# Performance work log

Measured on AMD Instinct MI355X. Metric: run time of the kernel, lower is better.

Reference implementation:

```python
import jax, jax.numpy as jnp
import numpy as np

NUM_NODES = 2   # number of iResNet blocks
H = 256         # internal_size
L = 4           # num_internal_layers (hidden Linear+ELU layers)
D = 2           # inp_size_linear (2D uv coords)
N = 1048576     # number of points (flattened 1024x1024 STMap grid)


def setup_inputs() -> dict:
    key = jax.random.key(0)
    ks = jax.random.split(key, 7)
    scale = 0.8 / np.sqrt(H)  # mimic lipschitz_correction (spectral norm <= 0.8)
    uv = jax.random.normal(ks[0], (N, D), jnp.float32)
    w_in = jax.random.normal(ks[1], (NUM_NODES, D, H), jnp.float32) * (0.8 / np.sqrt(D))
    b_in = jax.random.normal(ks[2], (NUM_NODES, H), jnp.float32) * 0.01
    w_hid = jax.random.normal(ks[3], (NUM_NODES, L, H, H), jnp.float32) * scale
    b_hid = jax.random.normal(ks[4], (NUM_NODES, L, H), jnp.float32) * 0.01
    w_out = jax.random.normal(ks[5], (NUM_NODES, H, D), jnp.float32) * scale
    b_out = jax.random.normal(ks[6], (NUM_NODES, D), jnp.float32) * 0.01
    return {"uv": uv, "w_in": w_in, "b_in": b_in, "w_hid": w_hid,
            "b_hid": b_hid, "w_out": w_out, "b_out": b_out}


def reference(uv, w_in, b_in, w_hid, b_hid, w_out, b_out):
    # Chain of NUM_NODES invertible ResNet blocks (forward / sensor_to_frustum):
    #   x <- x + MLP(x),  MLP = Lin(D,H)+ELU, L x (Lin(H,H)+ELU), Lin(H,D)
    x = uv  # [N, D]
    for i in range(NUM_NODES):
        h = jax.nn.elu(x @ w_in[i] + b_in[i])          # [N, H]
        for l in range(L):
            h = jax.nn.elu(h @ w_hid[i, l] + b_hid[i, l])
        x = x + (h @ w_out[i] + b_out[i])              # residual add, [N, D]
    return x
```

## Files before the change

kernel.cpp:

```cpp
#include <hip/hip_runtime.h>
#include <stdint.h>

typedef short bf16x8 __attribute__((ext_vector_type(8)));
typedef float f32x16 __attribute__((ext_vector_type(16)));
typedef float f32x4  __attribute__((ext_vector_type(4)));
typedef float f32x2  __attribute__((ext_vector_type(2)));

#define NODES  2
#define LAYERS 4
#define HD     256
#define MTILE  256
#define GRPB   8192
#define NGRP   (NODES*LAYERS*16)

__device__ __forceinline__ unsigned short f2bf(float f) {
  unsigned u = __float_as_uint(f);
  u += 0x7fffu + ((u >> 16) & 1u);
  return (unsigned short)(u >> 16);
}
__device__ __forceinline__ float bf2f(unsigned short s) {
  return __uint_as_float(((unsigned)s) << 16);
}
__device__ __forceinline__ float elu1(float v) {
  return v > 0.0f ? v : (__expf(v) - 1.0f);
}
__device__ __forceinline__ unsigned cvtpk(float lo, float hi) {
  unsigned r;
  asm("v_cvt_pk_bf16_f32 %0, %1, %2" : "=v"(r) : "v"(lo), "v"(hi));
  return r;
}
union U8 { bf16x8 v; unsigned u[4]; };

__global__ __launch_bounds__(256) void convw_kernel(const float* __restrict__ w_hid,
                                                    unsigned short* __restrict__ blob) {
  int e = blockIdx.x * 256 + threadIdx.x;
  int nl = e >> 16;
  int k  = (e >> 8) & 255;
  int n  = e & 255;
  float v = w_hid[(nl * 256 + k) * 256 + n];
  int qq  = k >> 6;
  int kc  = (k >> 4) & 3;
  int k16 = k & 15;
  int g   = (k16 >> 2) & 1;
  int i   = (k16 & 3) | ((k16 >> 3) << 2);
  int nf  = n >> 5, l31 = n & 31;
  unsigned boff = ((unsigned)(nl * 4 + qq) << 15)
                + ((unsigned)kc << 13) + ((unsigned)g << 12)
                + ((unsigned)nf << 9) + ((unsigned)l31 << 4) + ((unsigned)i << 1);
  blob[boff >> 1] = f2bf(v);
}

struct HG { bf16x8 a, b, c, d; };

__device__ __forceinline__ HG load_hg(const char* __restrict__ p) {
  HG r;
  r.a = *(const bf16x8*)(p);
  r.b = *(const bf16x8*)(p + 512);
  r.c = *(const bf16x8*)(p + 1024);
  r.d = *(const bf16x8*)(p + 1536);
  return r;
}

#define MM(af, h, accv) accv = __builtin_amdgcn_mfma_f32_32x32x16_bf16(af, h, accv, 0, 0, 0)

__global__ __launch_bounds__(256, 1) void nld_kernel(
    const float* __restrict__ uv, const float* __restrict__ w_in,
    const float* __restrict__ b_in, const float* __restrict__ b_hid,
    const float* __restrict__ w_out, const float* __restrict__ b_out,
    const unsigned short* __restrict__ blob, float* __restrict__ out, int nrows) {

  __shared__ __attribute__((aligned(16))) float pb_hid[NODES * LAYERS * HD];
  __shared__ __attribute__((aligned(16))) float pb_in[NODES * HD];

  const int t    = threadIdx.x;
  const int lane = t & 63;
  const int wv   = t >> 6;
  const int l31  = lane & 31;
  const int g    = lane >> 5;
  const long row0 = (long)blockIdx.x * MTILE + wv * 64 + l31;
  const long row1 = row0 + 32;

  for (int i = t; i < NODES * LAYERS * HD; i += 256) pb_hid[i] = b_hid[i];
  for (int i = t; i < NODES * HD; i += 256) pb_in[i] = b_in[i];

  float x00 = 0.f, x01 = 0.f, x10 = 0.f, x11 = 0.f;
  if (row0 < nrows) { f32x2 u = *(const f32x2*)(uv + row0 * 2); x00 = u[0]; x01 = u[1]; }
  if (row1 < nrows) { f32x2 u = *(const f32x2*)(uv + row1 * 2); x10 = u[0]; x11 = u[1]; }
  __syncthreads();

  bf16x8 hb0[16], hb1[16];
  const unsigned voff = (unsigned)(g * 4096 + l31 * 16);
  const char* gp   = (const char*)blob;
  const char* gend = (const char*)blob + (size_t)(NGRP - 1) * GRPB;

  HG A = load_hg(gp + voff);

  for (int nd = 0; nd < NODES; ++nd) {
    {
      const float* wi0 = w_in + nd * 2 * HD;
      const float* wi1 = wi0 + HD;
      const float* bi  = &pb_in[nd * HD];
#pragma unroll
      for (int c = 0; c < 16; ++c) {
        int kb = 16 * c + 4 * g;
        f32x4 a0 = *(const f32x4*)(wi0 + kb);
        f32x4 a1 = *(const f32x4*)(wi0 + kb + 8);
        f32x4 c0 = *(const f32x4*)(wi1 + kb);
        f32x4 c1 = *(const f32x4*)(wi1 + kb + 8);
        f32x4 e0 = *(const f32x4*)(bi + kb);
        f32x4 e1 = *(const f32x4*)(bi + kb + 8);
        float p0[8], p1[8];
#pragma unroll
        for (int j = 0; j < 4; ++j) {
          p0[j]     = elu1(fmaf(x01, c0[j], fmaf(x00, a0[j], e0[j])));
          p0[4 + j] = elu1(fmaf(x01, c1[j], fmaf(x00, a1[j], e1[j])));
          p1[j]     = elu1(fmaf(x11, c0[j], fmaf(x10, a0[j], e0[j])));
          p1[4 + j] = elu1(fmaf(x11, c1[j], fmaf(x10, a1[j], e1[j])));
        }
        U8 q0, q1;
        q0.u[0] = cvtpk(p0[0], p0[1]); q0.u[1] = cvtpk(p0[2], p0[3]);
        q0.u[2] = cvtpk(p0[4], p0[5]); q0.u[3] = cvtpk(p0[6], p0[7]);
        q1.u[0] = cvtpk(p1[0], p1[1]); q1.u[1] = cvtpk(p1[2], p1[3]);
        q1.u[2] = cvtpk(p1[4], p1[5]); q1.u[3] = cvtpk(p1[6], p1[7]);
        hb0[c] = q0.v;
        hb1[c] = q1.v;
      }
    }

    for (int ly = 0; ly < LAYERS; ++ly) {
      const float* bl = &pb_hid[(nd * LAYERS + ly) * HD];
      f32x16 acc0[8], acc1[8];
#pragma unroll
      for (int nf = 0; nf < 8; ++nf) {
        int nb = 32 * nf + 4 * g;
        f32x4 b0 = *(const f32x4*)(bl + nb);
        f32x4 b1 = *(const f32x4*)(bl + nb + 8);
        f32x4 b2 = *(const f32x4*)(bl + nb + 16);
        f32x4 b3 = *(const f32x4*)(bl + nb + 24);
#pragma unroll
        for (int j = 0; j < 4; ++j) {
          acc0[nf][j]      = b0[j]; acc1[nf][j]      = b0[j];
          acc0[nf][4 + j]  = b1[j]; acc1[nf][4 + j]  = b1[j];
          acc0[nf][8 + j]  = b2[j]; acc1[nf][8 + j]  = b2[j];
          acc0[nf][12 + j] = b3[j]; acc1[nf][12 + j] = b3[j];
        }
      }

#pragma unroll
      for (int u = 0; u < 16; ++u) {
        HG B = load_hg(gp + voff + 2048);
        bf16x8 h0 = hb0[u], h1 = hb1[u];
        MM(A.a, h0, acc0[0]); MM(A.a, h1, acc1[0]);
        MM(A.b, h0, acc0[1]); MM(A.b, h1, acc1[1]);
        MM(A.c, h0, acc0[2]); MM(A.c, h1, acc1[2]);
        MM(A.d, h0, acc0[3]); MM(A.d, h1, acc1[3]);
        const char* nx = gp + GRPB;
        if (nx > gend) nx = gend;
        A = load_hg(nx + voff);
        MM(B.a, h0, acc0[4]); MM(B.a, h1, acc1[4]);
        MM(B.b, h0, acc0[5]); MM(B.b, h1, acc1[5]);
        MM(B.c, h0, acc0[6]); MM(B.c, h1, acc1[6]);
        MM(B.d, h0, acc0[7]); MM(B.d, h1, acc1[7]);
        gp = nx;
      }

#pragma unroll
      for (int nf = 0; nf < 8; ++nf) {
        float e0[16], e1[16];
#pragma unroll
        for (int j = 0; j < 16; ++j) { e0[j] = elu1(acc0[nf][j]); e1[j] = elu1(acc1[nf][j]); }
        U8 p, q, r, s;
        p.u[0] = cvtpk(e0[0],  e0[1]);  p.u[1] = cvtpk(e0[2],  e0[3]);
        p.u[2] = cvtpk(e0[4],  e0[5]);  p.u[3] = cvtpk(e0[6],  e0[7]);
        q.u[0] = cvtpk(e0[8],  e0[9]);  q.u[1] = cvtpk(e0[10], e0[11]);
        q.u[2] = cvtpk(e0[12], e0[13]); q.u[3] = cvtpk(e0[14], e0[15]);
        r.u[0] = cvtpk(e1[0],  e1[1]);  r.u[1] = cvtpk(e1[2],  e1[3]);
        r.u[2] = cvtpk(e1[4],  e1[5]);  r.u[3] = cvtpk(e1[6],  e1[7]);
        s.u[0] = cvtpk(e1[8],  e1[9]);  s.u[1] = cvtpk(e1[10], e1[11]);
        s.u[2] = cvtpk(e1[12], e1[13]); s.u[3] = cvtpk(e1[14], e1[15]);
        hb0[2 * nf] = p.v; hb0[2 * nf + 1] = q.v;
        hb1[2 * nf] = r.v; hb1[2 * nf + 1] = s.v;
      }
    }

    {
      const float* wo = w_out + nd * HD * 2;
      float s00 = 0.f, s01 = 0.f, s10 = 0.f, s11 = 0.f;
#pragma unroll
      for (int c = 0; c < 16; ++c) {
        int kb = 16 * c + 4 * g;
        f32x4 wA0 = *(const f32x4*)(wo + kb * 2);
        f32x4 wA1 = *(const f32x4*)(wo + kb * 2 + 4);
        f32x4 wB0 = *(const f32x4*)(wo + (kb + 8) * 2);
        f32x4 wB1 = *(const f32x4*)(wo + (kb + 8) * 2 + 4);
        bf16x8 h0 = hb0[c], h1 = hb1[c];
#pragma unroll
        for (int j = 0; j < 2; ++j) {
          float f0 = bf2f((unsigned short)h0[2 * j]),     g0 = bf2f((unsigned short)h1[2 * j]);
          float f1 = bf2f((unsigned short)h0[2 * j + 1]), g1 = bf2f((unsigned short)h1[2 * j + 1]);
          float f2 = bf2f((unsigned short)h0[2 * j + 4]), g2 = bf2f((unsigned short)h1[2 * j + 4]);
          float f3 = bf2f((unsigned short)h0[2 * j + 5]), g3 = bf2f((unsigned short)h1[2 * j + 5]);
          const f32x4& wa = j ? wA1 : wA0;
          const f32x4& wbv = j ? wB1 : wB0;
          s00 = fmaf(f0, wa[0], s00);  s01 = fmaf(f0, wa[1], s01);
          s10 = fmaf(g0, wa[0], s10);  s11 = fmaf(g0, wa[1], s11);
          s00 = fmaf(f1, wa[2], s00);  s01 = fmaf(f1, wa[3], s01);
          s10 = fmaf(g1, wa[2], s10);  s11 = fmaf(g1, wa[3], s11);
          s00 = fmaf(f2, wbv[0], s00); s01 = fmaf(f2, wbv[1], s01);
          s10 = fmaf(g2, wbv[0], s10); s11 = fmaf(g2, wbv[1], s11);
          s00 = fmaf(f3, wbv[2], s00); s01 = fmaf(f3, wbv[3], s01);
          s10 = fmaf(g3, wbv[2], s10); s11 = fmaf(g3, wbv[3], s11);
        }
      }
      s00 += __shfl_xor(s00, 32); s01 += __shfl_xor(s01, 32);
      s10 += __shfl_xor(s10, 32); s11 += __shfl_xor(s11, 32);
      float bo0 = b_out[nd * 2 + 0], bo1 = b_out[nd * 2 + 1];
      x00 += s00 + bo0; x01 += s01 + bo1;
      x10 += s10 + bo0; x11 += s11 + bo1;
    }
  }

  if (g == 0) {
    if (row0 < nrows) { f32x2 r; r[0] = x00; r[1] = x01; *(f32x2*)(out + row0 * 2) = r; }
    if (row1 < nrows) { f32x2 r; r[0] = x10; r[1] = x11; *(f32x2*)(out + row1 * 2) = r; }
  }
}

extern "C" void kernel_launch(void* const* d_in, const int* in_sizes, int n_in,
                              void* d_out, int out_size, void* d_ws, size_t ws_size,
                              hipStream_t stream) {
  const float* uv    = (const float*)d_in[0];
  const float* w_in  = (const float*)d_in[1];
  const float* b_in  = (const float*)d_in[2];
  const float* w_hid = (const float*)d_in[3];
  const float* b_hid = (const float*)d_in[4];
  const float* w_out = (const float*)d_in[5];
  const float* b_out = (const float*)d_in[6];
  unsigned short* blob = (unsigned short*)d_ws;

  int whid_elems = in_sizes[3];
  convw_kernel<<<whid_elems / 256, 256, 0, stream>>>(w_hid, blob);

  int N = in_sizes[0] / 2;
  int grid = (N + MTILE - 1) / MTILE;
  nld_kernel<<<grid, 256, 0, stream>>>(uv, w_in, b_in, b_hid, w_out, b_out,
                                       blob, (float*)d_out, N);
}
```

Measured before the change: 1.266 ms.

## Stream weight chunks through LDS ring with async global-to-LDS loads

Replaces per-wave direct global loads of the bf16 weight fragments with a 6-slot LDS ring buffer. The block fills the ring using global_load_lds four chunks ahead and synchronises with waitcnt plus barrier, so each weight chunk is fetched once per block instead of once per wave. Block size drops from 256 to 128 threads, halving the tile, so more blocks run per CU and each has less redundant traffic. The cost is a barrier every k-chunk, LDS pressure, and inline waitcnt counting that must match the outstanding loads.

After: 1.441 ms. 1.14x slower.

```diff
diff --git a/kernel.cpp b/kernel.cpp
--- a/kernel.cpp
+++ b/kernel.cpp
@@ -9,9 +9,9 @@
 #define NODES  2
 #define LAYERS 4
 #define HD     256
-#define MTILE  256
-#define GRPB   8192
-#define NGRP   (NODES*LAYERS*16)
+#define MTILE  128
+#define CHB    8192
+#define NCH    (NODES*LAYERS*16)
 
 __device__ __forceinline__ unsigned short f2bf(float f) {
   unsigned u = __float_as_uint(f);
@@ -30,6 +30,13 @@
   return r;
 }
 union U8 { bf16x8 v; unsigned u[4]; };
+
+#define GLOAD_LDS16(gsrc, ldst)                                                        \
+  __builtin_amdgcn_global_load_lds(                                                    \
+      (const __attribute__((address_space(1))) unsigned int*)(gsrc),                   \
+      (__attribute__((address_space(3))) unsigned int*)(ldst), 16, 0, 0)
+
+#define MM(af, h, accv) accv = __builtin_amdgcn_mfma_f32_32x32x16_bf16(af, h, accv, 0, 0, 0)
 
 __global__ __launch_bounds__(256) void convw_kernel(const float* __restrict__ w_hid,
                                                     unsigned short* __restrict__ blob) {
@@ -50,25 +57,13 @@
   blob[boff >> 1] = f2bf(v);
 }
 
-struct HG { bf16x8 a, b, c, d; };
-
-__device__ __forceinline__ HG load_hg(const char* __restrict__ p) {
-  HG r;
-  r.a = *(const bf16x8*)(p);
-  r.b = *(const bf16x8*)(p + 512);
-  r.c = *(const bf16x8*)(p + 1024);
-  r.d = *(const bf16x8*)(p + 1536);
-  return r;
-}
-
-#define MM(af, h, accv) accv = __builtin_amdgcn_mfma_f32_32x32x16_bf16(af, h, accv, 0, 0, 0)
-
-__global__ __launch_bounds__(256, 1) void nld_kernel(
+__global__ __launch_bounds__(128, 1) void nld_kernel(
     const float* __restrict__ uv, const float* __restrict__ w_in,
     const float* __restrict__ b_in, const float* __restrict__ b_hid,
     const float* __restrict__ w_out, const float* __restrict__ b_out,
     const unsigned short* __restrict__ blob, float* __restrict__ out, int nrows) {
 
+  __shared__ __attribute__((aligned(16))) char  w_sm[6 * CHB];
   __shared__ __attribute__((aligned(16))) float pb_hid[NODES * LAYERS * HD];
   __shared__ __attribute__((aligned(16))) float pb_in[NODES * HD];
 
@@ -80,8 +75,21 @@
   const long row0 = (long)blockIdx.x * MTILE + wv * 64 + l31;
   const long row1 = row0 + 32;
 
-  for (int i = t; i < NODES * LAYERS * HD; i += 256) pb_hid[i] = b_hid[i];
-  for (int i = t; i < NODES * HD; i += 256) pb_in[i] = b_in[i];
+  const unsigned stoff = (unsigned)(t * 16);
+  const unsigned vfrag = (unsigned)(g * 4096 + l31 * 16);
+
+  auto stage = [&](int cs) {
+    const char* src = (const char*)blob + (size_t)cs * CHB + stoff;
+    char* dst = &w_sm[(unsigned)(cs % 6) * CHB + stoff];
+    GLOAD_LDS16(src,        dst);
+    GLOAD_LDS16(src + 2048, dst + 2048);
+    GLOAD_LDS16(src + 4096, dst + 4096);
+    GLOAD_LDS16(src + 6144, dst + 6144);
+  };
+
+  stage(0); stage(1); stage(2); stage(3);
+  for (int i = t; i < NODES * LAYERS * HD; i += 128) pb_hid[i] = b_hid[i];
+  for (int i = t; i < NODES * HD; i += 128) pb_in[i] = b_in[i];
 
   float x00 = 0.f, x01 = 0.f, x10 = 0.f, x11 = 0.f;
   if (row0 < nrows) { f32x2 u = *(const f32x2*)(uv + row0 * 2); x00 = u[0]; x01 = u[1]; }
@@ -89,11 +97,14 @@
   __syncthreads();
 
   bf16x8 hb0[16], hb1[16];
-  const unsigned voff = (unsigned)(g * 4096 + l31 * 16);
-  const char* gp   = (const char*)blob;
-  const char* gend = (const char*)blob + (size_t)(NGRP - 1) * GRPB;
-
-  HG A = load_hg(gp + voff);
+  bf16x8 wf0, wf1, wf2, wf3, wf4, wf5, wf6, wf7;
+  {
+    const char* wb = &w_sm[0] + vfrag;
+    wf0 = *(const bf16x8*)(wb + 0 * 512); wf1 = *(const bf16x8*)(wb + 1 * 512);
+    wf2 = *(const bf16x8*)(wb + 2 * 512); wf3 = *(const bf16x8*)(wb + 3 * 512);
+    wf4 = *(const bf16x8*)(wb + 4 * 512); wf5 = *(const bf16x8*)(wb + 5 * 512);
+    wf6 = *(const bf16x8*)(wb + 6 * 512); wf7 = *(const bf16x8*)(wb + 7 * 512);
+  }
 
   for (int nd = 0; nd < NODES; ++nd) {
     {
@@ -146,22 +157,35 @@
         }
       }
 
-#pragma unroll
-      for (int u = 0; u < 16; ++u) {
-        HG B = load_hg(gp + voff + 2048);
-        bf16x8 h0 = hb0[u], h1 = hb1[u];
-        MM(A.a, h0, acc0[0]); MM(A.a, h1, acc1[0]);
-        MM(A.b, h0, acc0[1]); MM(A.b, h1, acc1[1]);
-        MM(A.c, h0, acc0[2]); MM(A.c, h1, acc1[2]);
-        MM(A.d, h0, acc0[3]); MM(A.d, h1, acc1[3]);
-        const char* nx = gp + GRPB;
-        if (nx > gend) nx = gend;
-        A = load_hg(nx + voff);
-        MM(B.a, h0, acc0[4]); MM(B.a, h1, acc1[4]);
-        MM(B.b, h0, acc0[5]); MM(B.b, h1, acc1[5]);
-        MM(B.c, h0, acc0[6]); MM(B.c, h1, acc1[6]);
-        MM(B.d, h0, acc0[7]); MM(B.d, h1, acc1[7]);
-        gp = nx;
+      const int cbase = (nd * LAYERS + ly) * 16;
+#pragma unroll
+      for (int kc = 0; kc < 16; ++kc) {
+        const int c = cbase + kc;
+        asm volatile("s_waitcnt vmcnt(12)" ::: "memory");
+        __builtin_amdgcn_sched_barrier(0);
+        __builtin_amdgcn_s_barrier();
+        __builtin_amdgcn_sched_barrier(0);
+        int cs = c + 4; if (cs > NCH - 1) cs = NCH - 1;
+        stage(cs);
+        __builtin_amdgcn_sched_barrier(0);
+        bf16x8 h0 = hb0[kc], h1 = hb1[kc];
+        __builtin_amdgcn_s_setprio(1);
+        MM(wf0, h0, acc0[0]); MM(wf0, h1, acc1[0]);
+        MM(wf1, h0, acc0[1]); MM(wf1, h1, acc1[1]);
+        MM(wf2, h0, acc0[2]); MM(wf2, h1, acc1[2]);
+        MM(wf3, h0, acc0[3]); MM(wf3, h1, acc1[3]);
+        MM(wf4, h0, acc0[4]); MM(wf4, h1, acc1[4]);
+        MM(wf5, h0, acc0[5]); MM(wf5, h1, acc1[5]);
+        MM(wf6, h0, acc0[6]); MM(wf6, h1, acc1[6]);
+        MM(wf7, h0, acc0[7]); MM(wf7, h1, acc1[7]);
+        __builtin_amdgcn_s_setprio(0);
+        __builtin_amdgcn_sched_barrier(0);
+        int cn = c + 1; if (cn > NCH - 1) cn = NCH - 1;
+        const char* wb = &w_sm[(unsigned)(cn % 6) * CHB] + vfrag;
+        wf0 = *(const bf16x8*)(wb + 0 * 512); wf1 = *(const bf16x8*)(wb + 1 * 512);
+        wf2 = *(const bf16x8*)(wb + 2 * 512); wf3 = *(const bf16x8*)(wb + 3 * 512);
+        wf4 = *(const bf16x8*)(wb + 4 * 512); wf5 = *(const bf16x8*)(wb + 5 * 512);
+        wf6 = *(const bf16x8*)(wb + 6 * 512); wf7 = *(const bf16x8*)(wb + 7 * 512);
       }
 
 #pragma unroll
@@ -243,6 +267,6 @@
 
   int N = in_sizes[0] / 2;
   int grid = (N + MTILE - 1) / MTILE;
-  nld_kernel<<<grid, 256, 0, stream>>>(uv, w_in, b_in, b_hid, w_out, b_out,
+  nld_kernel<<<grid, 128, 0, stream>>>(uv, w_in, b_in, b_hid, w_out, b_out,
                                        blob, (float*)d_out, N);
 }
```
